# Performance work log

Measured on AMD Instinct MI355X. Metric: run time of the kernel, lower is better.

Reference implementation:

```python
import jax, jax.numpy as jnp
import numpy as np

HEADS = 8
DIM_HEAD = 64
SCALE = DIM_HEAD ** -0.5


def setup_inputs() -> dict:
    key = jax.random.key(0)
    ks = jax.random.split(key, 7)
    B, N, Dq = 2, 4096, 512
    M, Dc = 4096, 768
    inner = HEADS * DIM_HEAD  # 512
    x = jax.random.normal(ks[0], (B, N, Dq), dtype=jnp.float32)
    context = jax.random.normal(ks[1], (B, M, Dc), dtype=jnp.float32)
    # weights stored [in, out] (torch Linear weight transposed)
    Wq = jax.random.normal(ks[2], (Dq, inner), dtype=jnp.float32) * (Dq ** -0.5)
    Wk = jax.random.normal(ks[3], (Dc, inner), dtype=jnp.float32) * (Dc ** -0.5)
    Wv = jax.random.normal(ks[4], (Dc, inner), dtype=jnp.float32) * (Dc ** -0.5)
    Wo = jax.random.normal(ks[5], (inner, Dq), dtype=jnp.float32) * (inner ** -0.5)
    bo = jax.random.normal(ks[6], (Dq,), dtype=jnp.float32) * 0.01
    return {"x": x, "context": context, "Wq": Wq, "Wk": Wk, "Wv": Wv, "Wo": Wo, "bo": bo}


def reference(x, context, Wq, Wk, Wv, Wo, bo):
    B, N, _ = x.shape
    M = context.shape[1]
    h, d = HEADS, DIM_HEAD
    q = (x @ Wq).reshape(B, N, h, d)                      # b n h d
    k = ((context @ Wk) * SCALE).reshape(B, M, h, d)      # scale applied to k, as in source
    v = (context @ Wv).reshape(B, M, h, d)
    scores = jnp.einsum('bnhd,bmhd->bhnm', q, k)          # full QK^T
    attn = jax.nn.softmax(scores, axis=-1)
    out = jnp.einsum('bhnm,bmhd->bnhd', attn, v).reshape(B, N, h * d)
    return out @ Wo + bo  # dropout p=0.0 -> identity
```

## Files before the change

kernel.cpp:

```cpp
#include <hip/hip_runtime.h>

typedef unsigned short u16;
typedef __attribute__((ext_vector_type(4))) unsigned short u16x4;
typedef __attribute__((ext_vector_type(8))) unsigned short u16x8;
typedef __attribute__((ext_vector_type(8))) short s16x8;
typedef __attribute__((ext_vector_type(4))) float f32x4;
typedef __attribute__((ext_vector_type(16))) float f32x16;
typedef __attribute__((ext_vector_type(4))) unsigned int u32x4;

#define LOG2E 1.4426950408889634f

__device__ __forceinline__ u16 f2bf(float f) {
    return __builtin_bit_cast(unsigned short, static_cast<__bf16>(f));
}

__device__ __forceinline__ float bf2f(u16 v) {
    return __builtin_bit_cast(float, (unsigned)v << 16);
}

__device__ __forceinline__ float fexp2(float x) {
#if __has_builtin(__builtin_amdgcn_exp2f)
    return __builtin_amdgcn_exp2f(x);
#else
    return exp2f(x);
#endif
}

__device__ __forceinline__ s16x8 ld_frag(const u16* p) {
    return __builtin_bit_cast(s16x8, *reinterpret_cast<const u16x8*>(p));
}

__device__ __forceinline__ f32x4 mfma16(s16x8 a, s16x8 b, f32x4 c) {
    return __builtin_amdgcn_mfma_f32_16x16x32_bf16(a, b, c, 0, 0, 0);
}

__device__ __forceinline__ f32x16 mfma32(s16x8 a, s16x8 b, f32x16 c) {
    return __builtin_amdgcn_mfma_f32_32x32x16_bf16(a, b, c, 0, 0, 0);
}

__device__ __forceinline__ unsigned cvt_pk_bf16(float lo, float hi2) {
    unsigned r;
    asm("v_cvt_pk_bf16_f32 %0, %1, %2" : "=v"(r) : "v"(lo), "v"(hi2));
    return r;
}

__device__ __forceinline__ void plane32_swap(unsigned& x, unsigned& y) {
#if __has_builtin(__builtin_amdgcn_permlane32_swap)
    auto r = __builtin_amdgcn_permlane32_swap(x, y, false, false);
    x = r[0];
    y = r[1];
#else
    asm("v_permlane32_swap_b32 %0, %1" : "+v"(x), "+v"(y));
#endif
}

__device__ __forceinline__ void async16(const u16* g, u16* lds) {
    __builtin_amdgcn_global_load_lds(
        (__attribute__((address_space(1))) void*)const_cast<u16*>(g),
        (__attribute__((address_space(3))) void*)lds, 16, 0, 0);
}

__global__ __launch_bounds__(256) void prep_kernel(
    const float* __restrict__ x, const float* __restrict__ ctx, const float* __restrict__ Wq,
    const float* __restrict__ Wk, const float* __restrict__ Wv, const float* __restrict__ Wo,
    u16* __restrict__ xb, u16* __restrict__ cb, u16* __restrict__ Wqt, u16* __restrict__ Wkt,
    u16* __restrict__ Wvt, u16* __restrict__ Wot) {
    __shared__ float t[32][33];
    const int bidx = blockIdx.x;
    const int tid = threadIdx.x;
    if (bidx < 5120) {
        int i = bidx * 256 + tid;
        const float* in;
        u16* out;
        int idx;
        if (i < 524288) {
            in = x; out = xb; idx = i;
        } else {
            in = ctx; out = cb; idx = i - 524288;
        }
        const f32x4* p = (const f32x4*)in + ((size_t)idx << 1);
        f32x4 a = p[0], c = p[1];
        u16x8 v;
        v[0] = f2bf(a[0]); v[1] = f2bf(a[1]); v[2] = f2bf(a[2]); v[3] = f2bf(a[3]);
        v[4] = f2bf(c[0]); v[5] = f2bf(c[1]); v[6] = f2bf(c[2]); v[7] = f2bf(c[3]);
        *((u16x8*)out + idx) = v;
    } else {
        const int zb = bidx - 5120;
        const int z = zb / 384;
        const int rem = zb - z * 384;
        const int kx = rem % 24, ny = rem / 24;
        const float* W;
        u16* Wt;
        int Kd;
        float scale;
        switch (z) {
            case 0: W = Wq; Wt = Wqt; Kd = 512; scale = 1.0f; break;
            case 1: W = Wk; Wt = Wkt; Kd = 768; scale = 0.125f * LOG2E; break;
            case 2: W = Wv; Wt = Wvt; Kd = 768; scale = 1.0f; break;
            default: W = Wo; Wt = Wot; Kd = 512; scale = 1.0f; break;
        }
        const int k0 = kx << 5, n0 = ny << 5;
        if (k0 >= Kd) return;
        const int tx = tid & 31, ty = tid >> 5;
#pragma unroll
        for (int i = 0; i < 32; i += 8)
            t[ty + i][tx] = W[(size_t)(k0 + ty + i) * 512 + n0 + tx] * scale;
        __syncthreads();
#pragma unroll
        for (int i = 0; i < 32; i += 8)
            Wt[(size_t)(n0 + ty + i) * Kd + k0 + tx] = f2bf(t[tx][ty + i]);
    }
}

template <int MODE>
__device__ __forceinline__ void gemm_body(u16* __restrict__ Ab, u16* __restrict__ Bb,
                                          const u16* __restrict__ A, const u16* __restrict__ Bt,
                                          void* __restrict__ Cv, const float* __restrict__ bias,
                                          int K) {
    const int tid = threadIdx.x;
    const int w = tid >> 6, l = tid & 63;
    const int lg = l >> 4, lq = l & 15;
    const int wm = w >> 1, wn = w & 1;
    const int bm = blockIdx.y, bn = blockIdx.x;
    const int KT = K >> 6;

    f32x4 acc[4][4];
#pragma unroll
    for (int i = 0; i < 4; i++)
#pragma unroll
        for (int j = 0; j < 4; j++) acc[i][j] = (f32x4){0.f, 0.f, 0.f, 0.f};

    const u16* Ag0 = A + (size_t)bm * 128 * K;
    const u16* Bg0 = Bt + (size_t)bn * 128 * K;
    const int srow = l >> 3, scol = (l & 7) << 3;

    auto stage = [&](int kt, int buf) {
#pragma unroll
        for (int i = 0; i < 4; i++) {
            const int c = (w << 2) + i;
            const int row = (c << 3) + srow;
            async16(Ag0 + (size_t)row * K + kt * 64 + scol, Ab + (buf << 13) + (c << 9));
            async16(Bg0 + (size_t)row * K + kt * 64 + scol, Bb + (buf << 13) + (c << 9));
        }
    };

    stage(0, 0);
    for (int kt = 0; kt < KT; ++kt) {
        __syncthreads();
        if (kt + 1 < KT) stage(kt + 1, (kt + 1) & 1);
        const u16* As = Ab + ((kt & 1) << 13);
        const u16* Bs = Bb + ((kt & 1) << 13);
#pragma unroll
        for (int s = 0; s < 2; s++) {
            s16x8 af[4], bfr[4];
#pragma unroll
            for (int mt = 0; mt < 4; mt++)
                af[mt] = ld_frag(As + ((wm << 6) + (mt << 4) + lq) * 64 + (s << 5) + (lg << 3));
#pragma unroll
            for (int nt = 0; nt < 4; nt++)
                bfr[nt] = ld_frag(Bs + ((wn << 6) + (nt << 4) + lq) * 64 + (s << 5) + (lg << 3));
#pragma unroll
            for (int mt = 0; mt < 4; mt++)
#pragma unroll
                for (int nt = 0; nt < 4; nt++)
                    acc[mt][nt] = mfma16(af[mt], bfr[nt], acc[mt][nt]);
        }
    }
    const int row0 = bm * 128 + (wm << 6);
    const int col0 = bn * 128 + (wn << 6);
    if constexpr (MODE == 0) {
        u16* C = (u16*)Cv;
#pragma unroll
        for (int mt = 0; mt < 4; mt++)
#pragma unroll
            for (int nt = 0; nt < 4; nt++)
#pragma unroll
                for (int r = 0; r < 4; r++)
                    C[(size_t)(row0 + (mt << 4) + (lg << 2) + r) * 512 + col0 + (nt << 4) + lq] =
                        f2bf(acc[mt][nt][r]);
    } else if constexpr (MODE == 3) {
        float* C = (float*)Cv;
        float bv[4];
#pragma unroll
        for (int nt = 0; nt < 4; nt++) bv[nt] = bias[col0 + (nt << 4) + lq];
#pragma unroll
        for (int mt = 0; mt < 4; mt++)
#pragma unroll
            for (int nt = 0; nt < 4; nt++)
#pragma unroll
                for (int r = 0; r < 4; r++)
                    C[(size_t)(row0 + (mt << 4) + (lg << 2) + r) * 512 + col0 + (nt << 4) + lq] =
                        acc[mt][nt][r] + bv[nt];
    } else {
        u16* C = (u16*)Cv;
#pragma unroll
        for (int mt = 0; mt < 4; mt++)
#pragma unroll
            for (int nt = 0; nt < 4; nt++)
#pragma unroll
                for (int r = 0; r < 4; r++) {
                    const int m = row0 + (mt << 4) + (lg << 2) + r;
                    const int feat = col0 + (nt << 4) + lq;
                    const int bh = ((m >> 12) << 3) + (feat >> 6);
                    const int d = feat & 63;
                    const int kv = m & 4095;
                    const int T = kv >> 5, kvl = kv & 31;
                    size_t off;
                    if constexpr (MODE == 1) {
                        const int lane = kvl + (((d >> 3) & 1) << 5);
                        off = ((size_t)(((bh << 7) + T) << 2) + (d >> 4)) * 512 + (lane << 3) +
                              (d & 7);
                    } else {
                        const int lane = (d & 31) + (((kvl >> 3) & 1) << 5);
                        const int fi = ((kvl >> 4) << 1) + (d >> 5);
                        off = ((size_t)(((bh << 7) + T) << 2) + fi) * 512 + (lane << 3) +
                              (kvl & 7);
                    }
                    C[off] = f2bf(acc[mt][nt][r]);
                }
    }
}

__global__ __launch_bounds__(256, 2) void proj_gemm_kernel(
    const u16* __restrict__ xb, const u16* __restrict__ cb, const u16* __restrict__ Wqt,
    const u16* __restrict__ Wkt, const u16* __restrict__ Wvt, u16* __restrict__ Qb,
    u16* __restrict__ Kp, u16* __restrict__ Vp) {
    __shared__ u16 Ab[2][8192];
    __shared__ u16 Bb[2][8192];
    const int z = blockIdx.z;
    if (z == 0)
        gemm_body<0>(&Ab[0][0], &Bb[0][0], xb, Wqt, Qb, nullptr, 512);
    else if (z == 1)
        gemm_body<1>(&Ab[0][0], &Bb[0][0], cb, Wkt, Kp, nullptr, 768);
    else
        gemm_body<2>(&Ab[0][0], &Bb[0][0], cb, Wvt, Vp, nullptr, 768);
}

__global__ __launch_bounds__(256, 2) void out_gemm_kernel(const u16* __restrict__ Ob,
                                                          const u16* __restrict__ Wot,
                                                          float* __restrict__ out,
                                                          const float* __restrict__ bias) {
    __shared__ u16 Ab[2][8192];
    __shared__ u16 Bb[2][8192];
    gemm_body<3>(&Ab[0][0], &Bb[0][0], Ob, Wot, out, bias, 512);
}

__global__ __launch_bounds__(256, 4) void attn_kernel(const u16* __restrict__ Qb,
                                                      const u16* __restrict__ Kp,
                                                      const u16* __restrict__ Vp,
                                                      u16* __restrict__ Opart,
                                                      float* __restrict__ Lpart) {
    __shared__ u16 Kl[2][4096];
    __shared__ u16 Vl[2][4096];
    const int tid = threadIdx.x;
    const int w = tid >> 6, l = tid & 63;
    const int lq = l & 31, hi = l >> 5;
    const int bid = blockIdx.x;
    const int swz = ((bid & 7) << 8) + (bid >> 3);
    const int bh = swz >> 7, qtg = (swz >> 2) & 31, kvseg = swz & 3;
    const int qt = (qtg << 2) + w;
    const int wid = (((bh << 7) + qt) << 2) + kvseg;
    const int b = bh >> 3, h = bh & 7;

    const u16* Qp = Qb + (size_t)(b * 4096 + (qt << 5) + lq) * 512 + (h << 6) + (hi << 3);
    s16x8 qf[4];
#pragma unroll
    for (int s = 0; s < 4; s++) qf[s] = ld_frag(Qp + (s << 4));

    const u16* Kg = Kp + ((size_t)(bh << 7) + (kvseg << 5)) * 2048;
    const u16* Vg = Vp + ((size_t)(bh << 7) + (kvseg << 5)) * 2048;
    const int gsrc = (w << 9) + (l << 3);
    const int ldst = w << 9;
    const int roff = l << 3;

    f32x16 oacc0 = {}, oacc1 = {};
    float rs = 0.f;

    async16(Kg + gsrc, &Kl[0][ldst]);
    async16(Kg + 2048 + gsrc, &Kl[0][2048 + ldst]);
    async16(Vg + gsrc, &Vl[0][ldst]);
    async16(Vg + 2048 + gsrc, &Vl[0][2048 + ldst]);

    auto sub_body = [&](const u16* Kb_, const u16* Vb_) {
        s16x8 kf[4];
#pragma unroll
        for (int s = 0; s < 4; s++) kf[s] = ld_frag(Kb_ + (s << 9) + roff);
        f32x16 sacc = {};
        __builtin_amdgcn_s_setprio(1);
#pragma unroll
        for (int s = 0; s < 4; s++) sacc = mfma32(kf[s], qf[s], sacc);
        __builtin_amdgcn_s_setprio(0);

#pragma unroll
        for (int r = 0; r < 16; r++) sacc[r] = fexp2(sacc[r]);
        {
            float t0 = (sacc[0] + sacc[1]) + (sacc[2] + sacc[3]);
            float t1 = (sacc[4] + sacc[5]) + (sacc[6] + sacc[7]);
            float t2 = (sacc[8] + sacc[9]) + (sacc[10] + sacc[11]);
            float t3 = (sacc[12] + sacc[13]) + (sacc[14] + sacc[15]);
            rs += (t0 + t1) + (t2 + t3);
        }

        s16x8 aw[2];
#pragma unroll
        for (int sp = 0; sp < 2; sp++) {
            const int base2 = sp << 3;
            unsigned X1 = cvt_pk_bf16(sacc[base2 + 0], sacc[base2 + 1]);
            unsigned Y1 = cvt_pk_bf16(sacc[base2 + 4], sacc[base2 + 5]);
            unsigned X2 = cvt_pk_bf16(sacc[base2 + 2], sacc[base2 + 3]);
            unsigned Y2 = cvt_pk_bf16(sacc[base2 + 6], sacc[base2 + 7]);
            plane32_swap(X1, Y1);
            plane32_swap(X2, Y2);
            u32x4 wv;
            wv[0] = X1; wv[1] = X2; wv[2] = Y1; wv[3] = Y2;
            aw[sp] = __builtin_bit_cast(s16x8, wv);
        }

        s16x8 vf[4];
#pragma unroll
        for (int f = 0; f < 4; f++) vf[f] = ld_frag(Vb_ + (f << 9) + roff);
        __builtin_amdgcn_s_setprio(1);
#pragma unroll
        for (int sp = 0; sp < 2; sp++) {
            oacc0 = mfma32(aw[sp], vf[(sp << 1) + 0], oacc0);
            oacc1 = mfma32(aw[sp], vf[(sp << 1) + 1], oacc1);
        }
        __builtin_amdgcn_s_setprio(0);
    };

    for (int t = 0; t < 16; ++t) {
        const int buf = t & 1;
        __syncthreads();
        if (t + 1 < 16) {
            const size_t base = (size_t)(t + 1) * 4096;
            const int nb = buf ^ 1;
            async16(Kg + base + gsrc, &Kl[nb][ldst]);
            async16(Kg + base + 2048 + gsrc, &Kl[nb][2048 + ldst]);
            async16(Vg + base + gsrc, &Vl[nb][ldst]);
            async16(Vg + base + 2048 + gsrc, &Vl[nb][2048 + ldst]);
        }
        sub_body(&Kl[buf][0], &Vl[buf][0]);
        sub_body(&Kl[buf][2048], &Vl[buf][2048]);
    }

    u16* Ow = Opart + ((size_t)wid << 11);
#pragma unroll
    for (int r = 0; r < 16; r++) Ow[(r << 6) + l] = f2bf(oacc0[r]);
#pragma unroll
    for (int r = 0; r < 16; r++) Ow[((16 + r) << 6) + l] = f2bf(oacc1[r]);
    rs += __shfl_xor(rs, 32);
    if (l < 32) Lpart[(wid << 5) + l] = rs;
}

__global__ __launch_bounds__(256) void merge_kernel(const u16* __restrict__ Op,
                                                    const float* __restrict__ Lp,
                                                    u16* __restrict__ Ob) {
    const int g = blockIdx.x * 256 + threadIdx.x;
    const int slot = g >> 8;
    const int idx8 = (g & 255) << 3;
    const int dtr = idx8 >> 6;
    const int r = dtr & 15, dt = dtr >> 4;
    const int lane0 = idx8 & 63;
    const int q = (r & 3) + ((r >> 2) << 3) + ((lane0 >> 5) << 2);
    float lsum = 0.f;
#pragma unroll
    for (int p = 0; p < 4; p++) lsum += Lp[(slot << 7) + (p << 5) + q];
    const float ri = 1.f / lsum;
    float acc[8] = {0.f, 0.f, 0.f, 0.f, 0.f, 0.f, 0.f, 0.f};
#pragma unroll
    for (int p = 0; p < 4; p++) {
        const u16x8 a = *(const u16x8*)(Op + ((size_t)slot << 13) + (p << 11) + idx8);
#pragma unroll
        for (int j = 0; j < 8; j++) acc[j] += bf2f(a[j]);
    }
    u16x8 o;
#pragma unroll
    for (int j = 0; j < 8; j++) o[j] = f2bf(acc[j] * ri);
    const int bh = slot >> 7, qt = slot & 127;
    const int row = ((bh >> 3) << 12) + (qt << 5) + q;
    const int d = (lane0 & 31) + (dt << 5);
    *(u16x8*)(Ob + (size_t)row * 512 + ((bh & 7) << 6) + d) = o;
}

extern "C" void kernel_launch(void* const* d_in, const int* in_sizes, int n_in, void* d_out,
                              int out_size, void* d_ws, size_t ws_size, hipStream_t stream) {
    const float* x = (const float*)d_in[0];
    const float* ctx = (const float*)d_in[1];
    const float* Wq = (const float*)d_in[2];
    const float* Wk = (const float*)d_in[3];
    const float* Wv = (const float*)d_in[4];
    const float* Wo = (const float*)d_in[5];
    const float* bo = (const float*)d_in[6];
    float* out = (float*)d_out;

    char* ws = (char*)d_ws;
    u16* xb  = (u16*)(ws);
    u16* cb  = (u16*)(ws + 8388608);
    u16* Opart   = (u16*)(ws);
    float* Lpart = (float*)(ws + 33554432);
    u16* Qb  = (u16*)(ws + 34603008);
    u16* Ob  = (u16*)(ws + 34603008);
    u16* Kp  = (u16*)(ws + 42991616);
    u16* Vp  = (u16*)(ws + 51380224);
    u16* Wqt = (u16*)(ws + 59768832);
    u16* Wkt = (u16*)(ws + 60293120);
    u16* Wvt = (u16*)(ws + 61079552);
    u16* Wot = (u16*)(ws + 61865984);

    prep_kernel<<<dim3(6656), dim3(256), 0, stream>>>(x, ctx, Wq, Wk, Wv, Wo, xb, cb, Wqt, Wkt,
                                                      Wvt, Wot);
    proj_gemm_kernel<<<dim3(4, 64, 3), dim3(256), 0, stream>>>(xb, cb, Wqt, Wkt, Wvt, Qb, Kp, Vp);
    attn_kernel<<<dim3(2048), dim3(256), 0, stream>>>(Qb, Kp, Vp, Opart, Lpart);
    merge_kernel<<<dim3(2048), dim3(256), 0, stream>>>(Opart, Lpart, Ob);
    out_gemm_kernel<<<dim3(4, 64), dim3(256), 0, stream>>>(Ob, Wot, out, bo);
}
```

Measured before the change: 155.0 us.

## Stage K/V projection output in LDS for coalesced stores; interleave fragment loads with MFMAs

The K/V projection epilogue now writes the tile into shared memory in the attention-friendly packed layout. It then copies it out to global memory with contiguous 16-byte vector stores, replacing scattered 2-byte writes. In the attention inner loop, K and V fragment loads are double-buffered in two registers and interleaved with the MFMAs, instead of loading all four fragments up front. This lowers register pressure and overlaps LDS reads with matrix ops, at the cost of extra barriers in the GEMM epilogue and reliance on the compiler's scheduling.

Result: no change. 155.2 us (+0.1%).

```diff
diff --git a/kernel.cpp b/kernel.cpp
--- a/kernel.cpp
+++ b/kernel.cpp
@@ -192,7 +192,8 @@
                     C[(size_t)(row0 + (mt << 4) + (lg << 2) + r) * 512 + col0 + (nt << 4) + lq] =
                         acc[mt][nt][r] + bv[nt];
     } else {
-        u16* C = (u16*)Cv;
+        __syncthreads();
+        u16* Cl = Ab;
 #pragma unroll
         for (int mt = 0; mt < 4; mt++)
 #pragma unroll
@@ -200,24 +201,28 @@
 #pragma unroll
                 for (int r = 0; r < 4; r++) {
                     const int m = row0 + (mt << 4) + (lg << 2) + r;
-                    const int feat = col0 + (nt << 4) + lq;
-                    const int bh = ((m >> 12) << 3) + (feat >> 6);
-                    const int d = feat & 63;
-                    const int kv = m & 4095;
-                    const int T = kv >> 5, kvl = kv & 31;
-                    size_t off;
+                    const int d = (col0 + (nt << 4) + lq) & 63;
+                    const int kvl = m & 31;
+                    const int tl = (m >> 5) & 3;
+                    int op;
                     if constexpr (MODE == 1) {
-                        const int lane = kvl + (((d >> 3) & 1) << 5);
-                        off = ((size_t)(((bh << 7) + T) << 2) + (d >> 4)) * 512 + (lane << 3) +
-                              (d & 7);
+                        op = ((d >> 4) << 9) + ((kvl + (((d >> 3) & 1) << 5)) << 3) + (d & 7);
                     } else {
                         const int lane = (d & 31) + (((kvl >> 3) & 1) << 5);
                         const int fi = ((kvl >> 4) << 1) + (d >> 5);
-                        off = ((size_t)(((bh << 7) + T) << 2) + fi) * 512 + (lane << 3) +
-                              (kvl & 7);
+                        op = (fi << 9) + (lane << 3) + (kvl & 7);
                     }
-                    C[off] = f2bf(acc[mt][nt][r]);
+                    Cl[(((wn << 2) + tl) << 11) + op] = f2bf(acc[mt][nt][r]);
                 }
+        __syncthreads();
+        u16* C = (u16*)Cv;
+#pragma unroll
+        for (int c = 0; c < 8; c++) {
+            const int bhc = ((bm >> 5) << 3) + (bn << 1) + (c >> 2);
+            const int Tc = ((bm & 31) << 2) + (c & 3);
+            u16* dst = C + ((size_t)((bhc << 7) + Tc) << 11);
+            *(u16x8*)(dst + (tid << 3)) = *(const u16x8*)(Cl + (c << 11) + (tid << 3));
+        }
     }
 }
 
@@ -282,13 +287,16 @@
     async16(Vg + 2048 + gsrc, &Vl[0][2048 + ldst]);
 
     auto sub_body = [&](const u16* Kb_, const u16* Vb_) {
-        s16x8 kf[4];
-#pragma unroll
-        for (int s = 0; s < 4; s++) kf[s] = ld_frag(Kb_ + (s << 9) + roff);
         f32x16 sacc = {};
+        s16x8 fa = ld_frag(Kb_ + roff);
+        s16x8 fb = ld_frag(Kb_ + 512 + roff);
         __builtin_amdgcn_s_setprio(1);
-#pragma unroll
-        for (int s = 0; s < 4; s++) sacc = mfma32(kf[s], qf[s], sacc);
+        sacc = mfma32(fa, qf[0], sacc);
+        fa = ld_frag(Kb_ + 1024 + roff);
+        sacc = mfma32(fb, qf[1], sacc);
+        fb = ld_frag(Kb_ + 1536 + roff);
+        sacc = mfma32(fa, qf[2], sacc);
+        sacc = mfma32(fb, qf[3], sacc);
         __builtin_amdgcn_s_setprio(0);
 
 #pragma unroll
@@ -316,15 +324,15 @@
             aw[sp] = __builtin_bit_cast(s16x8, wv);
         }
 
-        s16x8 vf[4];
-#pragma unroll
-        for (int f = 0; f < 4; f++) vf[f] = ld_frag(Vb_ + (f << 9) + roff);
+        s16x8 va = ld_frag(Vb_ + roff);
+        s16x8 vb = ld_frag(Vb_ + 512 + roff);
         __builtin_amdgcn_s_setprio(1);
-#pragma unroll
-        for (int sp = 0; sp < 2; sp++) {
-            oacc0 = mfma32(aw[sp], vf[(sp << 1) + 0], oacc0);
-            oacc1 = mfma32(aw[sp], vf[(sp << 1) + 1], oacc1);
-        }
+        oacc0 = mfma32(aw[0], va, oacc0);
+        va = ld_frag(Vb_ + 1024 + roff);
+        oacc1 = mfma32(aw[0], vb, oacc1);
+        vb = ld_frag(Vb_ + 1536 + roff);
+        oacc0 = mfma32(aw[1], va, oacc0);
+        oacc1 = mfma32(aw[1], vb, oacc1);
         __builtin_amdgcn_s_setprio(0);
     };
 
```
